# Kernel optimization log

Measured on AMD Instinct MI355X. Metric: run time of the kernel, lower is better.

## Reference

```python
import jax, jax.numpy as jnp
import numpy as np

IN_CH = 512
NUM_HEADS = 8
DEPTH = IN_CH // NUM_HEADS
IN_FEAT = 37


def setup_inputs() -> dict:
    key = jax.random.key(0)
    ks = jax.random.split(key, 9)
    B, S = 4, 2048
    s_in = 1.0 / np.sqrt(IN_FEAT)
    s_ch = 1.0 / np.sqrt(IN_CH)
    return {
        "x": jax.random.normal(ks[0], (B, S, IN_FEAT), dtype=jnp.float32),
        "Wq": jax.random.uniform(ks[1], (IN_FEAT, IN_CH), jnp.float32, -s_in, s_in),
        "bq": jax.random.uniform(ks[2], (IN_CH,), jnp.float32, -s_in, s_in),
        "Wk": jax.random.uniform(ks[3], (IN_FEAT, IN_CH), jnp.float32, -s_in, s_in),
        "bk": jax.random.uniform(ks[4], (IN_CH,), jnp.float32, -s_in, s_in),
        "Wv": jax.random.uniform(ks[5], (IN_FEAT, IN_CH), jnp.float32, -s_in, s_in),
        "bv": jax.random.uniform(ks[6], (IN_CH,), jnp.float32, -s_in, s_in),
        "Wd": jax.random.uniform(ks[7], (IN_CH, IN_CH), jnp.float32, -s_ch, s_ch),
        "bd": jax.random.uniform(ks[8], (IN_CH,), jnp.float32, -s_ch, s_ch),
    }


def reference(x, Wq, bq, Wk, bk, Wv, bv, Wd, bd):
    B, S, _ = x.shape
    # projections: [B,S,in_ch] -> split into [B,S,H,D]
    q = (x @ Wq + bq).reshape(B, S, NUM_HEADS, DEPTH)
    k = (x @ Wk + bk).reshape(B, S, NUM_HEADS, DEPTH)
    v = (x @ Wv + bv).reshape(B, S, NUM_HEADS, DEPTH)
    scale = 1.0 / jnp.sqrt(jnp.float32(DEPTH))
    # scores: [B,H,Sq,Sk]
    logits = jnp.einsum("bqhd,bkhd->bhqk", q, k) * scale
    attn = jax.nn.softmax(logits, axis=-1)
    out = jnp.einsum("bhqk,bkhd->bqhd", attn, v).reshape(B, S, IN_CH)
    return out @ Wd + bd
```

## Files before the change

### kernel.cpp

```cpp
#include <hip/hip_runtime.h>
#include <hip/hip_bf16.h>
#include <stdint.h>

#define IN_FEAT 37
#define IN_CH 512
#define NUM_HEADS 8
#define DEPTH 64
#define BB 4
#define SS 2048
#define NROWS (BB * SS)

typedef unsigned short u16;
typedef __attribute__((ext_vector_type(8))) short bf16x8;
typedef __attribute__((ext_vector_type(4))) float f32x4;
typedef __attribute__((ext_vector_type(16))) float f32x16;
typedef __attribute__((ext_vector_type(4))) unsigned u32x4;

#define MFMA16(a, b, c) __builtin_amdgcn_mfma_f32_16x16x32_bf16(a, b, c, 0, 0, 0)
#define MFMA32(a, b, c) __builtin_amdgcn_mfma_f32_32x32x16_bf16(a, b, c, 0, 0, 0)

#define GLDS16(gsrc, ldst)                                                          \
    __builtin_amdgcn_global_load_lds(                                               \
        reinterpret_cast<const __attribute__((address_space(1))) void*>(            \
            reinterpret_cast<uintptr_t>(gsrc)),                                     \
        reinterpret_cast<__attribute__((address_space(3))) void*>(                  \
            reinterpret_cast<uintptr_t>(ldst)),                                     \
        16, 0, 0)

__device__ __forceinline__ u16 f2bf(float f) {
    union { float f; unsigned u; } v;
    v.f = f;
    unsigned r = v.u + 0x7fffu + ((v.u >> 16) & 1u);
    return (u16)(r >> 16);
}

__device__ __forceinline__ unsigned cvt_pk_bf16(float a, float b) {
    unsigned r;
    asm("v_cvt_pk_bf16_f32 %0, %1, %2" : "=v"(r) : "v"(a), "v"(b));
    return r;
}

__device__ __forceinline__ float fexp2(float x) {
    float r;
    asm("v_exp_f32 %0, %1" : "=v"(r) : "v"(x));
    return r;
}

#define XB_ELEMS (NROWS * 64)
#define WT_ELEMS (IN_CH * 64)
#define WD_ELEMS (IN_CH * IN_CH)
#define PACK_TOTAL (XB_ELEMS + 3 * WT_ELEMS + WD_ELEMS)

__global__ __launch_bounds__(256) void pack_all(
    const float* __restrict__ x,
    const float* __restrict__ Wq, const float* __restrict__ Wk,
    const float* __restrict__ Wv, const float* __restrict__ Wd,
    u16* __restrict__ xb, u16* __restrict__ WqT, u16* __restrict__ WkT,
    u16* __restrict__ WvT, u16* __restrict__ WdT)
{
    const float QSC = 0.125f * 1.44269504f;
    int idx = blockIdx.x * 256 + threadIdx.x;
    if (idx < XB_ELEMS) {
        int row = idx >> 6, col = idx & 63;
        xb[idx] = (col < IN_FEAT) ? f2bf(x[row * IN_FEAT + col]) : (u16)0;
    } else if (idx < XB_ELEMS + 3 * WT_ELEMS) {
        int j = idx - XB_ELEMS;
        int mat = j >> 15, rem = j & (WT_ELEMS - 1);
        int c = rem >> 6, i = rem & 63;
        float v = 0.f;
        if (i < IN_FEAT) {
            if (mat == 0)      v = Wq[i * IN_CH + c] * QSC;
            else if (mat == 1) v = Wk[i * IN_CH + c];
            else               v = Wv[i * IN_CH + c];
        }
        (mat == 0 ? WqT : mat == 1 ? WkT : WvT)[rem] = f2bf(v);
    } else if (idx < PACK_TOTAL) {
        int j = idx - (XB_ELEMS + 3 * WT_ELEMS);
        int r = j >> 9, c = j & 511;
        WdT[c * IN_CH + r] = f2bf(Wd[j]);
    }
}

__global__ __launch_bounds__(256) void proj_qk(
    const u16* __restrict__ xb, const u16* __restrict__ WqT,
    const u16* __restrict__ WkT, const float* __restrict__ bqp,
    const float* __restrict__ bkp, u16* __restrict__ qo, u16* __restrict__ ko)
{
    const float QSC = 0.125f * 1.44269504f;
    const int tid = threadIdx.x;
    const int w = tid >> 6, lane = tid & 63;
    const int g = lane >> 4, l15 = lane & 15;
    const int m0 = blockIdx.x * 64 + w * 16;
    const int n0 = blockIdx.y * 64;
    const f32x4 Z4 = {0.f, 0.f, 0.f, 0.f};

    f32x4 aq[4], ak[4];
#pragma unroll
    for (int nt = 0; nt < 4; ++nt) { aq[nt] = Z4; ak[nt] = Z4; }

#pragma unroll
    for (int k0 = 0; k0 < 64; k0 += 32) {
        bf16x8 a = *(const bf16x8*)&xb[(m0 + l15) * 64 + k0 + g * 8];
#pragma unroll
        for (int nt = 0; nt < 4; ++nt) {
            bf16x8 bq8 = *(const bf16x8*)&WqT[(n0 + nt * 16 + l15) * 64 + k0 + g * 8];
            bf16x8 bk8 = *(const bf16x8*)&WkT[(n0 + nt * 16 + l15) * 64 + k0 + g * 8];
            aq[nt] = MFMA16(a, bq8, aq[nt]);
            ak[nt] = MFMA16(a, bk8, ak[nt]);
        }
    }
#pragma unroll
    for (int nt = 0; nt < 4; ++nt) {
        const int n = n0 + nt * 16 + l15;
        const float bqv = bqp[n] * QSC, bkv = bkp[n];
        const int h = n >> 6, d = n & 63;
#pragma unroll
        for (int r = 0; r < 4; ++r) {
            const int m = m0 + g * 4 + r;
            const int b = m >> 11, s = m & 2047;
            const int bh = b * NUM_HEADS + h;
            qo[(bh * SS + s) * DEPTH + d] = f2bf(aq[nt][r] + bqv);
            ko[bh * (SS * 64) + (s >> 6) * 4096 + (s & 63) * 64 + (d ^ ((s & 7) << 3))] =
                f2bf(ak[nt][r] + bkv);
        }
    }
}

__global__ __launch_bounds__(256) void proj_vT(
    const u16* __restrict__ WvT, const u16* __restrict__ xb,
    const float* __restrict__ bvp, u16* __restrict__ vo)
{
    const int tid = threadIdx.x;
    const int w = tid >> 6, lane = tid & 63;
    const int g = lane >> 4, l15 = lane & 15;
    const int m0 = blockIdx.x * 64 + w * 16;
    const int n0 = blockIdx.y * 64;
    const f32x4 Z4 = {0.f, 0.f, 0.f, 0.f};

    f32x4 acc[4];
#pragma unroll
    for (int nt = 0; nt < 4; ++nt) acc[nt] = Z4;

#pragma unroll
    for (int k0 = 0; k0 < 64; k0 += 32) {
        bf16x8 a = *(const bf16x8*)&WvT[(m0 + l15) * 64 + k0 + g * 8];
#pragma unroll
        for (int nt = 0; nt < 4; ++nt) {
            bf16x8 b8 = *(const bf16x8*)&xb[(n0 + nt * 16 + l15) * 64 + k0 + g * 8];
            acc[nt] = MFMA16(a, b8, acc[nt]);
        }
    }
    float bvr[4];
#pragma unroll
    for (int r = 0; r < 4; ++r) bvr[r] = bvp[m0 + g * 4 + r];
#pragma unroll
    for (int nt = 0; nt < 4; ++nt) {
#pragma unroll
        for (int r = 0; r < 4; ++r) {
            const int c = m0 + g * 4 + r;
            const int rr = n0 + nt * 16 + l15;
            const int b = rr >> 11, s = rr & 2047;
            const int h = c >> 6, d = c & 63;
            const int bh = b * NUM_HEADS + h;
            vo[bh * (SS * 64) + (s >> 6) * 4096 + d * 64 + ((s & 63) ^ ((d & 7) << 3))] =
                f2bf(acc[nt][r] + bvr[r]);
        }
    }
}

#define NT (SS / 64)

__global__ __launch_bounds__(256, 4) void attn_kernel(
    const u16* __restrict__ Qm, const u16* __restrict__ Km,
    const u16* __restrict__ Vm, u16* __restrict__ Om)
{
    __shared__ u16 KL[4][2][2048];
    const int tid = threadIdx.x;
    const int w = tid >> 6, lane = tid & 63;
    const int r31 = lane & 31, lh = lane >> 5;
    const int qgrp = w >> 1, kh = w & 1;

    const int lin = blockIdx.x + gridDim.x * blockIdx.y;
    const int xcd = lin & 7, t7 = lin >> 3;
    const int bx = t7 & 31, bh = xcd + 8 * (t7 >> 5);
    const int qbase = bx * 64 + qgrp * 32;

    const u16* ktg = Km + bh * (SS * 64) + kh * 2048;
    const u16* vtg = Vm + bh * (SS * 64);

    bf16x8 Qf[4];
#pragma unroll
    for (int c = 0; c < 4; ++c)
        Qf[c] = *(const bf16x8*)&Qm[(bh * SS + qbase + r31) * 64 + c * 16 + lh * 8];

    f32x16 O0, O1, Z16;
#pragma unroll
    for (int i = 0; i < 16; ++i) { O0[i] = 0.f; O1[i] = 0.f; Z16[i] = 0.f; }
    float lreg = 0.f;

    auto STAGE_K = [&](int buf, int t) {
        const u16* ks = ktg + t * 4096 + lane * 8;
        u16* kd = &KL[w][buf][0];
#pragma unroll
        for (int i = 0; i < 4; ++i) GLDS16(ks + i * 512, kd + i * 512);
    };

    STAGE_K(0, 0);
    STAGE_K(1, 1);

    for (int t = 0; t < NT; ++t) {
        if (t < NT - 1) asm volatile("s_waitcnt vmcnt(4)" ::: "memory");
        else            asm volatile("s_waitcnt vmcnt(0)" ::: "memory");
        __builtin_amdgcn_sched_barrier(0);

        bf16x8 v[4];
        {
            const u16* vt = vtg + t * 4096;
#pragma unroll
            for (int dt = 0; dt < 2; ++dt)
#pragma unroll
                for (int o = 0; o < 2; ++o) {
                    const int vrow = dt * 32 + r31;
                    v[dt * 2 + o] = *(const bf16x8*)
                        &vt[vrow * 64 + ((kh * 32 + o * 16 + lh * 8) ^ ((vrow & 7) << 3))];
                }
        }

        const u16* kb = &KL[w][t & 1][0];
        bf16x8 kf[4];
#pragma unroll
        for (int c = 0; c < 4; ++c)
            kf[c] = *(const bf16x8*)&kb[r31 * 64 + ((c * 16 + lh * 8) ^ ((r31 & 7) << 3))];

        f32x16 s = MFMA32(kf[0], Qf[0], Z16);
        s = MFMA32(kf[1], Qf[1], s);
        s = MFMA32(kf[2], Qf[2], s);
        s = MFMA32(kf[3], Qf[3], s);

        if (t + 2 < NT) {
            asm volatile("s_waitcnt lgkmcnt(0)" ::: "memory");
            __builtin_amdgcn_sched_barrier(0);
            STAGE_K(t & 1, t + 2);
        }

        unsigned pk[8];
        float ps = 0.f;
#pragma unroll
        for (int j = 0; j < 8; ++j) {
            float a = fexp2(s[2 * j]);
            float b = fexp2(s[2 * j + 1]);
            ps += a + b;
            pk[j] = cvt_pk_bf16(a, b);
        }
        lreg += ps;

        asm("v_permlane32_swap_b32 %0, %1" : "+v"(pk[0]), "+v"(pk[2]));
        asm("v_permlane32_swap_b32 %0, %1" : "+v"(pk[1]), "+v"(pk[3]));
        asm("v_permlane32_swap_b32 %0, %1" : "+v"(pk[4]), "+v"(pk[6]));
        asm("v_permlane32_swap_b32 %0, %1" : "+v"(pk[5]), "+v"(pk[7]));

        union { u32x4 u; bf16x8 b; } f0, f1;
        f0.u = (u32x4){pk[0], pk[1], pk[2], pk[3]};
        f1.u = (u32x4){pk[4], pk[5], pk[6], pk[7]};

        O0 = MFMA32(f0.b, v[0], O0);
        O0 = MFMA32(f1.b, v[1], O0);
        O1 = MFMA32(f0.b, v[2], O1);
        O1 = MFMA32(f1.b, v[3], O1);
    }

    asm volatile("s_waitcnt vmcnt(0)" ::: "memory");
    __syncthreads();
    float lfull = lreg + __shfl_xor(lreg, 32, 64);
    float* sc = (float*)&KL[0][0][0];
    float* scp = sc + qgrp * 2112;
    if (kh == 1) {
#pragma unroll
        for (int i = 0; i < 16; ++i) scp[i * 64 + lane] = O0[i];
#pragma unroll
        for (int i = 0; i < 16; ++i) scp[(16 + i) * 64 + lane] = O1[i];
        scp[2048 + lane] = lfull;
    }
    __syncthreads();
    if (kh == 0) {
#pragma unroll
        for (int i = 0; i < 16; ++i) O0[i] += scp[i * 64 + lane];
#pragma unroll
        for (int i = 0; i < 16; ++i) O1[i] += scp[(16 + i) * 64 + lane];
        const float inv = 1.0f / (lfull + scp[2048 + lane]);
        const int b = bh >> 3, hh = bh & 7;
#pragma unroll
        for (int i = 0; i < 16; ++i) {
            const int qr = (i & 3) + 8 * (i >> 2) + 4 * lh;
            const float invq = __shfl(inv, qr, 64);
            const int srow = qbase + qr;
            u16* orow = &Om[((b * SS + srow) << 9) + hh * 64];
            orow[r31]      = f2bf(O0[i] * invq);
            orow[32 + r31] = f2bf(O1[i] * invq);
        }
    }
}

__global__ __launch_bounds__(256) void out_gemm(
    const u16* __restrict__ A, const u16* __restrict__ BT,
    const float* __restrict__ bd, float* __restrict__ out)
{
    const int tid = threadIdx.x;
    const int w = tid >> 6, lane = tid & 63;
    const int g = lane >> 4, l15 = lane & 15;
    const int m0 = blockIdx.x * 64 + w * 16;
    const int n0 = blockIdx.y * 64;
    const f32x4 Z4 = {0.f, 0.f, 0.f, 0.f};

    f32x4 acc[4];
#pragma unroll
    for (int nt = 0; nt < 4; ++nt) acc[nt] = Z4;

    for (int k0 = 0; k0 < IN_CH; k0 += 32) {
        bf16x8 a = *(const bf16x8*)&A[(m0 + l15) * IN_CH + k0 + g * 8];
#pragma unroll
        for (int nt = 0; nt < 4; ++nt) {
            bf16x8 b = *(const bf16x8*)&BT[(n0 + nt * 16 + l15) * IN_CH + k0 + g * 8];
            acc[nt] = MFMA16(a, b, acc[nt]);
        }
    }
#pragma unroll
    for (int nt = 0; nt < 4; ++nt)
#pragma unroll
        for (int r = 0; r < 4; ++r) {
            const int m = m0 + g * 4 + r;
            const int n = n0 + nt * 16 + l15;
            out[m * IN_CH + n] = acc[nt][r] + bd[n];
        }
}

extern "C" void kernel_launch(void* const* d_in, const int* in_sizes, int n_in,
                              void* d_out, int out_size, void* d_ws, size_t ws_size,
                              hipStream_t stream)
{
    const float* x  = (const float*)d_in[0];
    const float* Wq = (const float*)d_in[1];
    const float* bq = (const float*)d_in[2];
    const float* Wk = (const float*)d_in[3];
    const float* bk = (const float*)d_in[4];
    const float* Wv = (const float*)d_in[5];
    const float* bv = (const float*)d_in[6];
    const float* Wd = (const float*)d_in[7];
    const float* bd = (const float*)d_in[8];
    float* out = (float*)d_out;

    u16* ws  = (u16*)d_ws;
    u16* q   = ws;
    u16* k   = q + NROWS * IN_CH;
    u16* vT  = k + NROWS * IN_CH;
    u16* ao  = vT + NROWS * IN_CH;
    u16* WdT = ao + NROWS * IN_CH;
    u16* xb  = WdT + WD_ELEMS;
    u16* WqT = xb + XB_ELEMS;
    u16* WkT = WqT + WT_ELEMS;
    u16* WvT = WkT + WT_ELEMS;

    pack_all<<<dim3((PACK_TOTAL + 255) / 256), dim3(256), 0, stream>>>(
        x, Wq, Wk, Wv, Wd, xb, WqT, WkT, WvT, WdT);
    proj_qk<<<dim3(NROWS / 64, IN_CH / 64), dim3(256), 0, stream>>>(
        xb, WqT, WkT, bq, bk, q, k);
    proj_vT<<<dim3(IN_CH / 64, NROWS / 64), dim3(256), 0, stream>>>(
        WvT, xb, bv, vT);
    attn_kernel<<<dim3(SS / 64, BB * NUM_HEADS), dim3(256), 0, stream>>>(q, k, vT, ao);
    out_gemm<<<dim3(NROWS / 64, IN_CH / 64), dim3(256), 0, stream>>>(ao, WdT, bd, out);
}
```

Before: 123.8 us.

## Unroll attention loop by two and interleave QK, softmax and PV across tiles

The key-tile loop now processes two tiles per iteration. The second tile's QK MFMAs and V loads are issued while the first tile's exp/permlane work is in flight, and its exp runs after the first tile's PV MFMAs. The goal is to overlap VALU exponentials with matrix-core work. Both K buffers are restaged together after a full vmcnt(0) wait, so the prefetch distance drops from one tile-ahead streaming to batch refills, which may expose load latency. It also assumes NT is even and raises register pressure.

```diff
diff --git a/kernel.cpp b/kernel.cpp
--- a/kernel.cpp
+++ b/kernel.cpp
@@ -204,69 +204,98 @@
 #pragma unroll
         for (int i = 0; i < 4; ++i) GLDS16(ks + i * 512, kd + i * 512);
     };
-
-    STAGE_K(0, 0);
-    STAGE_K(1, 1);
-
-    for (int t = 0; t < NT; ++t) {
-        if (t < NT - 1) asm volatile("s_waitcnt vmcnt(4)" ::: "memory");
-        else            asm volatile("s_waitcnt vmcnt(0)" ::: "memory");
-        __builtin_amdgcn_sched_barrier(0);
-
-        bf16x8 v[4];
-        {
-            const u16* vt = vtg + t * 4096;
-#pragma unroll
-            for (int dt = 0; dt < 2; ++dt)
-#pragma unroll
-                for (int o = 0; o < 2; ++o) {
-                    const int vrow = dt * 32 + r31;
-                    v[dt * 2 + o] = *(const bf16x8*)
-                        &vt[vrow * 64 + ((kh * 32 + o * 16 + lh * 8) ^ ((vrow & 7) << 3))];
-                }
-        }
-
-        const u16* kb = &KL[w][t & 1][0];
+    auto VLOAD = [&](bf16x8 (&v)[4], int t) {
+        const u16* vt = vtg + t * 4096;
+#pragma unroll
+        for (int dt = 0; dt < 2; ++dt)
+#pragma unroll
+            for (int o = 0; o < 2; ++o) {
+                const int vrow = dt * 32 + r31;
+                v[dt * 2 + o] = *(const bf16x8*)
+                    &vt[vrow * 64 + ((kh * 32 + o * 16 + lh * 8) ^ ((vrow & 7) << 3))];
+            }
+    };
+    auto QK = [&](const u16* kb) -> f32x16 {
         bf16x8 kf[4];
 #pragma unroll
         for (int c = 0; c < 4; ++c)
             kf[c] = *(const bf16x8*)&kb[r31 * 64 + ((c * 16 + lh * 8) ^ ((r31 & 7) << 3))];
-
         f32x16 s = MFMA32(kf[0], Qf[0], Z16);
         s = MFMA32(kf[1], Qf[1], s);
         s = MFMA32(kf[2], Qf[2], s);
         s = MFMA32(kf[3], Qf[3], s);
-
-        if (t + 2 < NT) {
+        return s;
+    };
+
+    STAGE_K(0, 0);
+    STAGE_K(1, 1);
+
+#pragma unroll 1
+    for (int tt = 0; tt < NT; tt += 2) {
+        asm volatile("s_waitcnt vmcnt(0)" ::: "memory");
+        __builtin_amdgcn_sched_barrier(0);
+
+        bf16x8 vA[4];
+        VLOAD(vA, tt);
+
+        f32x16 sA = QK(&KL[w][0][0]);
+        unsigned pkA[8];
+        float psA = 0.f;
+#pragma unroll
+        for (int j = 0; j < 8; ++j) {
+            float a = fexp2(sA[2 * j]);
+            float b = fexp2(sA[2 * j + 1]);
+            psA += a + b;
+            pkA[j] = cvt_pk_bf16(a, b);
+        }
+        lreg += psA;
+        asm("v_permlane32_swap_b32 %0, %1" : "+v"(pkA[0]), "+v"(pkA[2]));
+        asm("v_permlane32_swap_b32 %0, %1" : "+v"(pkA[1]), "+v"(pkA[3]));
+        asm("v_permlane32_swap_b32 %0, %1" : "+v"(pkA[4]), "+v"(pkA[6]));
+        asm("v_permlane32_swap_b32 %0, %1" : "+v"(pkA[5]), "+v"(pkA[7]));
+        union { u32x4 u; bf16x8 b; } f0A, f1A;
+        f0A.u = (u32x4){pkA[0], pkA[1], pkA[2], pkA[3]};
+        f1A.u = (u32x4){pkA[4], pkA[5], pkA[6], pkA[7]};
+
+        f32x16 sB = QK(&KL[w][1][0]);
+
+        bf16x8 vB[4];
+        VLOAD(vB, tt + 1);
+
+        if (tt + 2 < NT) {
             asm volatile("s_waitcnt lgkmcnt(0)" ::: "memory");
             __builtin_amdgcn_sched_barrier(0);
-            STAGE_K(t & 1, t + 2);
-        }
-
-        unsigned pk[8];
-        float ps = 0.f;
+            STAGE_K(0, tt + 2);
+            STAGE_K(1, tt + 3);
+        }
+
+        O0 = MFMA32(f0A.b, vA[0], O0);
+        O0 = MFMA32(f1A.b, vA[1], O0);
+        O1 = MFMA32(f0A.b, vA[2], O1);
+        O1 = MFMA32(f1A.b, vA[3], O1);
+
+        unsigned pkB[8];
+        float psB = 0.f;
 #pragma unroll
         for (int j = 0; j < 8; ++j) {
-            float a = fexp2(s[2 * j]);
-            float b = fexp2(s[2 * j + 1]);
-            ps += a + b;
-            pk[j] = cvt_pk_bf16(a, b);
-        }
-        lreg += ps;
-
-        asm("v_permlane32_swap_b32 %0, %1" : "+v"(pk[0]), "+v"(pk[2]));
-        asm("v_permlane32_swap_b32 %0, %1" : "+v"(pk[1]), "+v"(pk[3]));
-        asm("v_permlane32_swap_b32 %0, %1" : "+v"(pk[4]), "+v"(pk[6]));
-        asm("v_permlane32_swap_b32 %0, %1" : "+v"(pk[5]), "+v"(pk[7]));
-
-        union { u32x4 u; bf16x8 b; } f0, f1;
-        f0.u = (u32x4){pk[0], pk[1], pk[2], pk[3]};
-        f1.u = (u32x4){pk[4], pk[5], pk[6], pk[7]};
-
-        O0 = MFMA32(f0.b, v[0], O0);
-        O0 = MFMA32(f1.b, v[1], O0);
-        O1 = MFMA32(f0.b, v[2], O1);
-        O1 = MFMA32(f1.b, v[3], O1);
+            float a = fexp2(sB[2 * j]);
+            float b = fexp2(sB[2 * j + 1]);
+            psB += a + b;
+            pkB[j] = cvt_pk_bf16(a, b);
+        }
+        lreg += psB;
+        asm("v_permlane32_swap_b32 %0, %1" : "+v"(pkB[0]), "+v"(pkB[2]));
+        asm("v_permlane32_swap_b32 %0, %1" : "+v"(pkB[1]), "+v"(pkB[3]));
+        asm("v_permlane32_swap_b32 %0, %1" : "+v"(pkB[4]), "+v"(pkB[6]));
+        asm("v_permlane32_swap_b32 %0, %1" : "+v"(pkB[5]), "+v"(pkB[7]));
+        union { u32x4 u; bf16x8 b; } f0B, f1B;
+        f0B.u = (u32x4){pkB[0], pkB[1], pkB[2], pkB[3]};
+        f1B.u = (u32x4){pkB[4], pkB[5], pkB[6], pkB[7]};
+
+        O0 = MFMA32(f0B.b, vB[0], O0);
+        O0 = MFMA32(f1B.b, vB[1], O0);
+        O1 = MFMA32(f0B.b, vB[2], O1);
+        O1 = MFMA32(f1B.b, vB[3], O1);
     }
 
     asm volatile("s_waitcnt vmcnt(0)" ::: "memory");
```

After: 162.2 us. 31.0% more time.
